# Performance work log

Measured on AMD Instinct MI355X. Metric: run time of the kernel, lower is better.

The kernel has to match this reference:

```python
import jax, jax.numpy as jnp
import numpy as np

B, T, E, H = 8, 2048, 1024, 1024  # batch, seq, embed, head size

def setup_inputs() -> dict:
    key = jax.random.key(0)
    k1, k2, k3, k4 = jax.random.split(key, 4)
    x = jax.random.normal(k1, (B, T, E), dtype=jnp.float32)
    # torch nn.Linear weights are [out, in]; scale down for stability
    Wk = jax.random.normal(k2, (H, E), dtype=jnp.float32) * (E ** -0.5)
    Wq = jax.random.normal(k3, (H, E), dtype=jnp.float32) * (E ** -0.5)
    Wv = jax.random.normal(k4, (H, E), dtype=jnp.float32) * (E ** -0.5)
    return {"x": x, "Wk": Wk, "Wq": Wq, "Wv": Wv}

def reference(x, Wk, Wq, Wv):
    Bx, Tx, Ex = x.shape
    k = jnp.einsum('bte,he->bth', x, Wk)   # [B,T,H]
    q = jnp.einsum('bte,he->bth', x, Wq)
    v = jnp.einsum('bte,he->bth', x, Wv)
    # NOTE: original scales by embed_dim**-0.5 (z = input last dim), not head size
    scores = jnp.einsum('bth,bsh->bts', q, k) * (Ex ** -0.5)  # [B,T,T]
    causal = jnp.tril(jnp.ones((Tx, Tx), dtype=bool))
    scores = jnp.where(causal, scores, -jnp.inf)
    wei = jax.nn.softmax(scores, axis=-1)
    return jnp.einsum('bts,bsh->bth', wei, v)
```

## Files before the change

kernel.cpp:

```cpp
#include <hip/hip_runtime.h>
#include <hip/hip_bf16.h>

typedef unsigned short u16;
typedef __bf16 bf16x8 __attribute__((ext_vector_type(8)));
typedef unsigned short u16x8 __attribute__((ext_vector_type(8)));
typedef unsigned short u16x4 __attribute__((ext_vector_type(4)));
typedef float f32x4 __attribute__((ext_vector_type(4)));

#define B_ 8
#define T_ 2048
#define E_ 1024
#define H_ 1024
#define M_ (B_ * T_)

__device__ inline u16 f2bf(float f) {
    __bf16 h = (__bf16)f;
    return __builtin_bit_cast(u16, h);
}

__device__ inline bf16x8 load_frag(const u16* p) {
    u16x8 u = *(const u16x8*)p;
    return __builtin_bit_cast(bf16x8, u);
}

__device__ inline void gload_lds16(const u16* g, u16* l) {
    __builtin_amdgcn_global_load_lds(
        (__attribute__((address_space(1))) unsigned int*)(g),
        (__attribute__((address_space(3))) unsigned int*)(l), 16, 0, 0);
}

__global__ void castk(const float* __restrict__ in, u16* __restrict__ out, int n) {
    int i = (blockIdx.x * blockDim.x + threadIdx.x) * 4;
    if (i < n) {
        f32x4 f = *(const f32x4*)(in + i);
        u16x4 u;
        u[0] = f2bf(f[0]); u[1] = f2bf(f[1]); u[2] = f2bf(f[2]); u[3] = f2bf(f[3]);
        *(u16x4*)(out + i) = u;
    }
}

__global__ __launch_bounds__(256) void gemm_qkv(const u16* __restrict__ A,
                                                const u16* __restrict__ W,
                                                u16* __restrict__ qo,
                                                u16* __restrict__ ko,
                                                u16* __restrict__ vo) {
    const int bm = blockIdx.x, bn = blockIdx.y;
    const int tid = threadIdx.x;
    const int w = tid >> 6, lane = tid & 63, quad = lane >> 4, l16 = lane & 15;
    const int wr = w & 1, wc = w >> 1;

    __shared__ u16 As[128 * 64];
    __shared__ u16 Bs[128 * 64];

    f32x4 acc[16] = {};

    const u16* Ab = A + (size_t)(bm * 128) * E_;
    const u16* Wb = W + (size_t)(bn * 128) * E_;

    for (int kk = 0; kk < E_; kk += 64) {
        __syncthreads();
#pragma unroll
        for (int i = 0; i < 4; i++) {
            int chunk = i * 256 + tid;
            int row = chunk >> 3, cc = chunk & 7;
            int ccs = cc ^ (row & 7);
            gload_lds16(Ab + (size_t)row * E_ + kk + ccs * 8, &As[chunk * 8]);
            gload_lds16(Wb + (size_t)row * E_ + kk + ccs * 8, &Bs[chunk * 8]);
        }
        __syncthreads();
#pragma unroll
        for (int k2 = 0; k2 < 2; k2++) {
            bf16x8 af[4], bf[4];
#pragma unroll
            for (int ri = 0; ri < 4; ri++) {
                int m = wr * 64 + ri * 16 + l16;
                int slot = m * 8 + ((k2 * 4 + quad) ^ (m & 7));
                af[ri] = load_frag(&As[slot * 8]);
            }
#pragma unroll
            for (int ci = 0; ci < 4; ci++) {
                int n = wc * 64 + ci * 16 + l16;
                int slot = n * 8 + ((k2 * 4 + quad) ^ (n & 7));
                bf[ci] = load_frag(&Bs[slot * 8]);
            }
#pragma unroll
            for (int ri = 0; ri < 4; ri++)
#pragma unroll
                for (int ci = 0; ci < 4; ci++)
                    acc[ri * 4 + ci] = __builtin_amdgcn_mfma_f32_16x16x32_bf16(
                        af[ri], bf[ci], acc[ri * 4 + ci], 0, 0, 0);
        }
    }

    const int nbase = bn * 128;
#pragma unroll
    for (int ri = 0; ri < 4; ri++) {
#pragma unroll
        for (int ci = 0; ci < 4; ci++) {
#pragma unroll
            for (int r = 0; r < 4; r++) {
                int row = bm * 128 + wr * 64 + ri * 16 + quad * 4 + r;
                int n = nbase + wc * 64 + ci * 16 + l16;
                u16 v = f2bf(acc[ri * 4 + ci][r]);
                if (n < 1024) {
                    qo[(size_t)row * H_ + n] = v;
                } else if (n < 2048) {
                    ko[(size_t)row * H_ + (n - 1024)] = v;
                } else {
                    int b = row >> 11, t = row & (T_ - 1);
                    vo[((size_t)b * H_ + (n - 2048)) * T_ + t] = v;
                }
            }
        }
    }
}

#define INF __builtin_inff()
__global__ __launch_bounds__(512, 2) void attn(const u16* __restrict__ qb,
                                               const u16* __restrict__ kb,
                                               const u16* __restrict__ vtb,
                                               float* __restrict__ out) {
    const int b = blockIdx.y;
    const int t0 = ((int)gridDim.x - 1 - (int)blockIdx.x) * 64;
    const int tid = threadIdx.x;
    const int w = tid >> 6, lane = tid & 63, quad = lane >> 4, l16 = lane & 15;
    const int srow = tid >> 3, sg = tid & 7;

    __shared__ u16 Qs[64 * 1024];
    __shared__ float Ssm[64 * 128];

    u16* P = (u16*)Ssm;
    float* a_s = (float*)((char*)Ssm + 64 * 136 * 2);

    const u16* qB = qb + (size_t)b * T_ * H_;
    const u16* kB = kb + (size_t)b * T_ * H_;
    const u16* vB = vtb + (size_t)b * H_ * T_;
    const float scale = 0.03125f;

#pragma unroll
    for (int i = 0; i < 16; i++) {
        int s = i * 512 + tid;
        int row = s >> 7, c2 = s & 127;
        int cc = c2 ^ (row & 7);
        gload_lds16(qB + (size_t)(t0 + row) * H_ + cc * 8, &Qs[s * 8]);
    }

    float m_r = -INF, l_r = 0.f;
    f32x4 o[32] = {};

    __syncthreads();

    for (int s0 = 0; s0 <= t0 + 63; s0 += 128) {
        f32x4 sc[4] = {};
        {
            const u16* kp = kB + (size_t)(s0 + w * 16 + l16) * H_ + quad * 8;
#pragma unroll 2
            for (int kk = 0; kk < H_; kk += 32) {
                bf16x8 kf = load_frag(kp + kk);
                int kc8 = (kk >> 3) + quad;
#pragma unroll
                for (int mt = 0; mt < 4; mt++) {
                    int row = mt * 16 + l16;
                    int slot = row * 128 + (kc8 ^ (row & 7));
                    bf16x8 af = load_frag(&Qs[slot * 8]);
                    sc[mt] = __builtin_amdgcn_mfma_f32_16x16x32_bf16(af, kf, sc[mt], 0, 0, 0);
                }
            }
        }
        __syncthreads();
        {
            int col = w * 16 + l16;
            int g = col >> 2, cl = col & 3;
#pragma unroll
            for (int mt = 0; mt < 4; mt++) {
#pragma unroll
                for (int r = 0; r < 4; r++) {
                    int row = mt * 16 + quad * 4 + r;
                    int g2 = g ^ (row & 7);
                    Ssm[row * 128 + g2 * 4 + cl] =
                        (s0 + col <= t0 + row) ? sc[mt][r] * scale : -INF;
                }
            }
        }
        __syncthreads();

        float vv[16];
#pragma unroll
        for (int i4 = 0; i4 < 4; i4++) {
            int g2 = (sg * 4 + i4) ^ (srow & 7);
            f32x4 t = *(const f32x4*)&Ssm[srow * 128 + g2 * 4];
            vv[i4 * 4 + 0] = t[0]; vv[i4 * 4 + 1] = t[1];
            vv[i4 * 4 + 2] = t[2]; vv[i4 * 4 + 3] = t[3];
        }
        float rmax = vv[0];
#pragma unroll
        for (int i = 1; i < 16; i++) rmax = fmaxf(rmax, vv[i]);
#pragma unroll
        for (int off = 4; off >= 1; off >>= 1) rmax = fmaxf(rmax, __shfl_xor(rmax, off, 64));
        float mn = fmaxf(m_r, rmax);
        float alpha = __expf(m_r - mn);
        float rsum = 0.f;
        u16x8 pl, ph;
#pragma unroll
        for (int i = 0; i < 8; i++) {
            float p = __expf(vv[i] - mn);
            rsum += p; pl[i] = f2bf(p);
        }
#pragma unroll
        for (int i = 0; i < 8; i++) {
            float p = __expf(vv[8 + i] - mn);
            rsum += p; ph[i] = f2bf(p);
        }
#pragma unroll
        for (int off = 4; off >= 1; off >>= 1) rsum += __shfl_xor(rsum, off, 64);
        l_r = l_r * alpha + rsum;
        m_r = mn;
        __syncthreads();
        *(u16x8*)&P[srow * 136 + sg * 16] = pl;
        *(u16x8*)&P[srow * 136 + sg * 16 + 8] = ph;
        if (sg == 0) a_s[srow] = alpha;
        __syncthreads();

        {
#pragma unroll
            for (int mt = 0; mt < 4; mt++) {
#pragma unroll
                for (int r = 0; r < 4; r++) {
                    float al = a_s[mt * 16 + quad * 4 + r];
#pragma unroll
                    for (int ht = 0; ht < 8; ht++) o[mt * 8 + ht][r] *= al;
                }
            }
            const u16* vp = vB + (size_t)(w * 128 + l16) * T_ + s0 + quad * 8;
#pragma unroll
            for (int kc = 0; kc < 4; kc++) {
                bf16x8 pa[4];
#pragma unroll
                for (int mt = 0; mt < 4; mt++)
                    pa[mt] = load_frag(&P[(mt * 16 + l16) * 136 + kc * 32 + quad * 8]);
#pragma unroll
                for (int ht = 0; ht < 8; ht++) {
                    bf16x8 vf = load_frag(vp + (size_t)ht * 16 * T_ + kc * 32);
#pragma unroll
                    for (int mt = 0; mt < 4; mt++)
                        o[mt * 8 + ht] = __builtin_amdgcn_mfma_f32_16x16x32_bf16(
                            pa[mt], vf, o[mt * 8 + ht], 0, 0, 0);
                }
            }
        }
    }

    __syncthreads();
    if (sg == 0) a_s[srow] = l_r;
    __syncthreads();
    float* ob = out + (size_t)b * T_ * H_;
#pragma unroll
    for (int mt = 0; mt < 4; mt++) {
#pragma unroll
        for (int r = 0; r < 4; r++) {
            float linv = 1.f / a_s[mt * 16 + quad * 4 + r];
            int row = t0 + mt * 16 + quad * 4 + r;
#pragma unroll
            for (int ht = 0; ht < 8; ht++) {
                int col = w * 128 + ht * 16 + l16;
                ob[(size_t)row * H_ + col] = o[mt * 8 + ht][r] * linv;
            }
        }
    }
}

extern "C" void kernel_launch(void* const* d_in, const int* in_sizes, int n_in,
                              void* d_out, int out_size, void* d_ws, size_t ws_size,
                              hipStream_t stream) {
    const float* x  = (const float*)d_in[0];
    const float* Wk = (const float*)d_in[1];
    const float* Wq = (const float*)d_in[2];
    const float* Wv = (const float*)d_in[3];
    float* out = (float*)d_out;

    char* ws = (char*)d_ws;
    const size_t SZ_XB  = (size_t)M_ * E_ * 2;
    const size_t SZ_W   = (size_t)3 * H_ * E_ * 2;
    const size_t SZ_QKV = (size_t)M_ * H_ * 2;
    u16* xb   = (u16*)(ws);
    u16* wqkv = (u16*)(ws + SZ_XB);
    u16* qb   = (u16*)(ws + SZ_XB + SZ_W);
    u16* kb   = (u16*)(ws + SZ_XB + SZ_W + SZ_QKV);
    u16* vtb  = (u16*)(ws + SZ_XB + SZ_W + 2 * SZ_QKV);

    castk<<<M_ * E_ / 4 / 256, 256, 0, stream>>>(x, xb, M_ * E_);
    castk<<<H_ * E_ / 4 / 256, 256, 0, stream>>>(Wq, wqkv, H_ * E_);
    castk<<<H_ * E_ / 4 / 256, 256, 0, stream>>>(Wk, wqkv + (size_t)H_ * E_, H_ * E_);
    castk<<<H_ * E_ / 4 / 256, 256, 0, stream>>>(Wv, wqkv + (size_t)2 * H_ * E_, H_ * E_);

    gemm_qkv<<<dim3(M_ / 128, 3072 / 128), 256, 0, stream>>>(xb, wqkv, qb, kb, vtb);

    attn<<<dim3(T_ / 64, B_), 512, 0, stream>>>(qb, kb, vtb, out);
}
```

Baseline: 560.7 us.

## Store K and V in MFMA fragment-ordered layout and stage GEMM epilogue through LDS

The QKV GEMM epilogue now writes its tile into shared memory with a swizzle and then emits 16-byte vector stores. Q stays row-major, while K and V go into a pre-tiled layout where every MFMA fragment is one contiguous 512-element block. The attention kernel reads K and V fragments as fully coalesced lane*8 loads instead of strided row loads. Each wave in the QK^T stage now computes a 2x2 block of 16x16 tiles, which reuses each Q fragment across two K fragments. The intent is to cut uncoalesced scattered 2-byte stores, especially the transposed V writes, and to improve global load efficiency in attention, at the cost of an extra LDS round trip and more complex indexing.

Measured after the change: 612.1 us. +9.2%, slower.

```diff
diff --git a/kernel.cpp b/kernel.cpp
--- a/kernel.cpp
+++ b/kernel.cpp
@@ -49,8 +49,9 @@
     const int w = tid >> 6, lane = tid & 63, quad = lane >> 4, l16 = lane & 15;
     const int wr = w & 1, wc = w >> 1;
 
-    __shared__ u16 As[128 * 64];
-    __shared__ u16 Bs[128 * 64];
+    __shared__ u16 smem[128 * 128];
+    u16* As = smem;
+    u16* Bs = smem + 128 * 64;
 
     f32x4 acc[16] = {};
 
@@ -92,33 +93,73 @@
         }
     }
 
-    const int nbase = bn * 128;
-#pragma unroll
-    for (int ri = 0; ri < 4; ri++) {
-#pragma unroll
-        for (int ci = 0; ci < 4; ci++) {
-#pragma unroll
-            for (int r = 0; r < 4; r++) {
-                int row = bm * 128 + wr * 64 + ri * 16 + quad * 4 + r;
-                int n = nbase + wc * 64 + ci * 16 + l16;
-                u16 v = f2bf(acc[ri * 4 + ci][r]);
-                if (n < 1024) {
-                    qo[(size_t)row * H_ + n] = v;
-                } else if (n < 2048) {
-                    ko[(size_t)row * H_ + (n - 1024)] = v;
-                } else {
-                    int b = row >> 11, t = row & (T_ - 1);
-                    vo[((size_t)b * H_ + (n - 2048)) * T_ + t] = v;
+    __syncthreads();
+    if (bn < 16) {
+#pragma unroll
+        for (int ri = 0; ri < 4; ri++)
+#pragma unroll
+            for (int ci = 0; ci < 4; ci++) {
+                int n = wc * 64 + ci * 16 + l16;
+#pragma unroll
+                for (int r = 0; r < 4; r++) {
+                    int m = wr * 64 + ri * 16 + quad * 4 + r;
+                    smem[m * 128 + (((n >> 3) ^ (m & 15)) << 3) + (n & 7)] =
+                        f2bf(acc[ri * 4 + ci][r]);
                 }
             }
+    } else {
+#pragma unroll
+        for (int ri = 0; ri < 4; ri++)
+#pragma unroll
+            for (int ci = 0; ci < 4; ci++) {
+                int n = wc * 64 + ci * 16 + l16;
+                int m0 = wr * 64 + ri * 16 + quad * 4;
+                u16x4 pk;
+#pragma unroll
+                for (int r = 0; r < 4; r++) pk[r] = f2bf(acc[ri * 4 + ci][r]);
+                *(u16x4*)&smem[n * 128 + (((m0 >> 3) ^ (n & 15)) << 3) + (m0 & 7)] = pk;
+            }
+    }
+    __syncthreads();
+
+    const int b = bm >> 4;
+    if (bn < 8) {
+#pragma unroll
+        for (int i = 0; i < 8; i++) {
+            int c = i * 256 + tid;
+            int m = c >> 4, nc = c & 15;
+            u16x8 v = *(u16x8*)&smem[m * 128 + ((nc ^ (m & 15)) << 3)];
+            *(u16x8*)&qo[(size_t)(bm * 128 + m) * H_ + bn * 128 + nc * 8] = v;
+        }
+    } else if (bn < 16) {
+#pragma unroll
+        for (int i = 0; i < 8; i++) {
+            int c = i * 256 + tid;
+            int si = c & 15, q = (c >> 4) & 3, hbl = (c >> 6) & 3, stl = c >> 8;
+            int m = stl * 16 + si, nch = hbl * 4 + q;
+            u16x8 v = *(u16x8*)&smem[m * 128 + ((nch ^ (m & 15)) << 3)];
+            int stile = (bm & 15) * 8 + stl;
+            int hb = (bn - 8) * 4 + hbl;
+            *(u16x8*)&ko[(((size_t)b * 128 + stile) * 32 + hb) * 512 + q * 128 + si * 8] = v;
+        }
+    } else {
+#pragma unroll
+        for (int i = 0; i < 8; i++) {
+            int c = i * 256 + tid;
+            int hi = c & 15, q = (c >> 4) & 3, sbl = (c >> 6) & 3, hbl = c >> 8;
+            int nl = hbl * 16 + hi, mch = sbl * 4 + q;
+            u16x8 v = *(u16x8*)&smem[nl * 128 + ((mch ^ (nl & 15)) << 3)];
+            int hb = (bn - 16) * 8 + hbl;
+            int sb = (bm & 15) * 4 + sbl;
+            *(u16x8*)&vo[(((size_t)b * 64 + hb) * 64 + sb) * 512 + q * 128 + hi * 8] = v;
         }
     }
 }
 
 #define INF __builtin_inff()
 __global__ __launch_bounds__(512, 2) void attn(const u16* __restrict__ qb,
-                                               const u16* __restrict__ kb,
-                                               const u16* __restrict__ vtb,
+                                               const u16* __restrict__ kfg,
+                                               const u16* __restrict__ vfg,
                                                float* __restrict__ out) {
     const int b = blockIdx.y;
     const int t0 = ((int)gridDim.x - 1 - (int)blockIdx.x) * 64;
@@ -133,8 +174,8 @@
     float* a_s = (float*)((char*)Ssm + 64 * 136 * 2);
 
     const u16* qB = qb + (size_t)b * T_ * H_;
-    const u16* kB = kb + (size_t)b * T_ * H_;
-    const u16* vB = vtb + (size_t)b * H_ * T_;
+    const u16* kfB = kfg + (size_t)b * 2097152;
+    const u16* vfB = vfg + (size_t)b * 2097152;
     const float scale = 0.03125f;
 
 #pragma unroll
@@ -147,40 +188,42 @@
 
     float m_r = -INF, l_r = 0.f;
     f32x4 o[32] = {};
+    const int mg = (w & 1) * 32, cg = (w >> 1) * 32;
 
     __syncthreads();
 
     for (int s0 = 0; s0 <= t0 + 63; s0 += 128) {
-        f32x4 sc[4] = {};
+        f32x4 sc[2][2] = {{{}, {}}, {{}, {}}};
         {
-            const u16* kp = kB + (size_t)(s0 + w * 16 + l16) * H_ + quad * 8;
+            const u16* kp0 = kfB + ((size_t)((s0 >> 4) + (w >> 1) * 2) * 32) * 512 + lane * 8;
 #pragma unroll 2
             for (int kk = 0; kk < H_; kk += 32) {
-                bf16x8 kf = load_frag(kp + kk);
+                bf16x8 kf0 = load_frag(kp0 + kk * 16);
+                bf16x8 kf1 = load_frag(kp0 + 16384 + kk * 16);
                 int kc8 = (kk >> 3) + quad;
 #pragma unroll
-                for (int mt = 0; mt < 4; mt++) {
-                    int row = mt * 16 + l16;
-                    int slot = row * 128 + (kc8 ^ (row & 7));
-                    bf16x8 af = load_frag(&Qs[slot * 8]);
-                    sc[mt] = __builtin_amdgcn_mfma_f32_16x16x32_bf16(af, kf, sc[mt], 0, 0, 0);
+                for (int mt2 = 0; mt2 < 2; mt2++) {
+                    int row = mg + mt2 * 16 + l16;
+                    bf16x8 af = load_frag(&Qs[(row * 128 + (kc8 ^ (row & 7))) * 8]);
+                    sc[mt2][0] = __builtin_amdgcn_mfma_f32_16x16x32_bf16(af, kf0, sc[mt2][0], 0, 0, 0);
+                    sc[mt2][1] = __builtin_amdgcn_mfma_f32_16x16x32_bf16(af, kf1, sc[mt2][1], 0, 0, 0);
                 }
             }
         }
         __syncthreads();
         {
-            int col = w * 16 + l16;
-            int g = col >> 2, cl = col & 3;
-#pragma unroll
-            for (int mt = 0; mt < 4; mt++) {
-#pragma unroll
-                for (int r = 0; r < 4; r++) {
-                    int row = mt * 16 + quad * 4 + r;
-                    int g2 = g ^ (row & 7);
-                    Ssm[row * 128 + g2 * 4 + cl] =
-                        (s0 + col <= t0 + row) ? sc[mt][r] * scale : -INF;
-                }
-            }
+#pragma unroll
+            for (int mt2 = 0; mt2 < 2; mt2++)
+#pragma unroll
+                for (int ct2 = 0; ct2 < 2; ct2++)
+#pragma unroll
+                    for (int r = 0; r < 4; r++) {
+                        int row = mg + mt2 * 16 + quad * 4 + r;
+                        int col = cg + ct2 * 16 + l16;
+                        int g2 = (col >> 2) ^ (row & 7);
+                        Ssm[row * 128 + g2 * 4 + (col & 3)] =
+                            (s0 + col <= t0 + row) ? sc[mt2][ct2][r] * scale : -INF;
+                    }
         }
         __syncthreads();
 
@@ -231,7 +274,7 @@
                     for (int ht = 0; ht < 8; ht++) o[mt * 8 + ht][r] *= al;
                 }
             }
-            const u16* vp = vB + (size_t)(w * 128 + l16) * T_ + s0 + quad * 8;
+            const u16* vpb = vfB + ((size_t)(s0 >> 5)) * 512 + lane * 8;
 #pragma unroll
             for (int kc = 0; kc < 4; kc++) {
                 bf16x8 pa[4];
@@ -240,11 +283,11 @@
                     pa[mt] = load_frag(&P[(mt * 16 + l16) * 136 + kc * 32 + quad * 8]);
 #pragma unroll
                 for (int ht = 0; ht < 8; ht++) {
-                    bf16x8 vf = load_frag(vp + (size_t)ht * 16 * T_ + kc * 32);
+                    bf16x8 vfr = load_frag(vpb + (size_t)(w * 8 + ht) * 32768 + kc * 512);
 #pragma unroll
                     for (int mt = 0; mt < 4; mt++)
                         o[mt * 8 + ht] = __builtin_amdgcn_mfma_f32_16x16x32_bf16(
-                            pa[mt], vf, o[mt * 8 + ht], 0, 0, 0);
+                            pa[mt], vfr, o[mt * 8 + ht], 0, 0, 0);
                 }
             }
         }
@@ -285,15 +328,15 @@
     u16* xb   = (u16*)(ws);
     u16* wqkv = (u16*)(ws + SZ_XB);
     u16* qb   = (u16*)(ws + SZ_XB + SZ_W);
-    u16* kb   = (u16*)(ws + SZ_XB + SZ_W + SZ_QKV);
-    u16* vtb  = (u16*)(ws + SZ_XB + SZ_W + 2 * SZ_QKV);
+    u16* kfb  = (u16*)(ws + SZ_XB + SZ_W + SZ_QKV);
+    u16* vfb  = (u16*)(ws + SZ_XB + SZ_W + 2 * SZ_QKV);
 
     castk<<<M_ * E_ / 4 / 256, 256, 0, stream>>>(x, xb, M_ * E_);
     castk<<<H_ * E_ / 4 / 256, 256, 0, stream>>>(Wq, wqkv, H_ * E_);
     castk<<<H_ * E_ / 4 / 256, 256, 0, stream>>>(Wk, wqkv + (size_t)H_ * E_, H_ * E_);
     castk<<<H_ * E_ / 4 / 256, 256, 0, stream>>>(Wv, wqkv + (size_t)2 * H_ * E_, H_ * E_);
 
-    gemm_qkv<<<dim3(M_ / 128, 3072 / 128), 256, 0, stream>>>(xb, wqkv, qb, kb, vtb);
-
-    attn<<<dim3(T_ / 64, B_), 512, 0, stream>>>(qb, kb, vtb, out);
-}
+    gemm_qkv<<<dim3(M_ / 128, 3072 / 128), 256, 0, stream>>>(xb, wqkv, qb, kfb, vfb);
+
+    attn<<<dim3(T_ / 64, B_), 512, 0, stream>>>(qb, kfb, vfb, out);
+}
```
